# Optimization experiments

Hardware: AMD Instinct MI355X
Metric: run time of the kernel (lower is better)

The kernel has to match this reference:

```python
import jax, jax.numpy as jnp
import numpy as np

N = 100000
E = 1600000
B = 4
IN_C, HID_C, OUT_C = 128, 16, 64
EPS = 1e-5


def _xavier(key, shape):
    fan_in, fan_out = shape[0], shape[1]
    a = float(np.sqrt(6.0 / (fan_in + fan_out)))
    return jax.random.uniform(key, shape, jnp.float32, -a, a)


def setup_inputs() -> dict:
    key = jax.random.key(0)
    ks = jax.random.split(key, 12)
    return {
        "X": jax.random.normal(ks[0], (B, N, IN_C), jnp.float32),
        "edge_index0": jax.random.randint(ks[1], (2, E), 0, N, jnp.int32),
        "edge_weight0": jax.random.uniform(ks[2], (E,), jnp.float32),
        "edge_index1": jax.random.randint(ks[3], (2, E), 0, N, jnp.int32),
        "edge_weight1": jax.random.uniform(ks[4], (E,), jnp.float32),
        "n_id": jnp.arange(N, dtype=jnp.int32),
        "res_n_id0": jnp.arange(N, dtype=jnp.int32),
        "res_n_id1": jnp.arange(N, dtype=jnp.int32),
        # layer 1 params
        "W1_1": _xavier(ks[5], (IN_C, HID_C)),
        "W2_1": _xavier(ks[6], (1, HID_C)),
        "U1": _xavier(ks[7], (HID_C, HID_C)),
        "V1": _xavier(ks[8], (HID_C, HID_C)),
        # layer 2 params
        "W1_2": _xavier(ks[9], (HID_C, OUT_C)),
        "W2_2": _xavier(ks[10], (1, OUT_C)),
        "U2": _xavier(ks[11], (OUT_C, OUT_C)),
        "V2": _xavier(jax.random.fold_in(key, 99), (OUT_C, OUT_C)),
    }


def gated_gcn(x, edge_index, edge_weight, res_n_id, W1, W2, U, V, n_dst):
    # x: [B, N_src, C_in]
    x = x @ W1                                   # [B, N_src, C]
    edge_emb = edge_weight[:, None] * W2[0]      # [E, C]  (edge_feature @ W2)
    src, dst = edge_index[0], edge_index[1]
    msg = edge_emb[None, :, :] * (x[:, src, :] @ V)          # [B, E, C]
    # scatter-mean over destination nodes
    sums = jax.ops.segment_sum(jnp.swapaxes(msg, 0, 1), dst,
                               num_segments=n_dst)            # [N_dst, B, C]
    cnt = jax.ops.segment_sum(jnp.ones((msg.shape[1],), msg.dtype), dst,
                              num_segments=n_dst)
    aggr = jnp.swapaxes(sums, 0, 1) / jnp.maximum(cnt, 1.0)[None, :, None]
    # update
    xr = x[:, res_n_id, :]                       # [B, N_dst, C]
    a = xr @ U + aggr
    # fresh BatchNorm1d(num_features=N_dst) in train mode: normalize each
    # node index over (batch, channel); affine is identity (gamma=1, beta=0)
    mean = jnp.mean(a, axis=(0, 2), keepdims=True)
    var = jnp.var(a, axis=(0, 2), keepdims=True)
    a = jax.nn.relu((a - mean) * jax.lax.rsqrt(var + EPS))
    return xr + a


def reference(X, edge_index0, edge_weight0, edge_index1, edge_weight1,
              n_id, res_n_id0, res_n_id1,
              W1_1, W2_1, U1, V1, W1_2, W2_2, U2, V2):
    X = X[:, n_id, :]
    X = gated_gcn(X, edge_index0, edge_weight0, res_n_id0,
                  W1_1, W2_1, U1, V1, N)
    X = gated_gcn(X, edge_index1, edge_weight1, res_n_id1,
                  W1_2, W2_2, U2, V2, N)
    return X
```

## Files before the change

kernel.cpp:

```cpp
#include <hip/hip_runtime.h>

#define NN 100000
#define EE 1600000
#define EPS 1e-5f
#define NBUK 391
#define NB1 782

typedef __attribute__((ext_vector_type(8))) short short8;
typedef __attribute__((ext_vector_type(4))) float floatx4;
union FragU { uint u[4]; short8 s; };

__device__ __forceinline__ ushort f2bf(float f) {
    uint u = __float_as_uint(f);
    uint r = (u + 0x7FFF + ((u >> 16) & 1)) >> 16;
    return (ushort)r;
}
__device__ __forceinline__ float bf2f(ushort u) {
    return __uint_as_float(((uint)u) << 16);
}

__global__ __launch_bounds__(256) void prep(const float* __restrict__ W1_1,
                                            const float* __restrict__ U1,
                                            const float* __restrict__ V1,
                                            const float* __restrict__ W2_1,
                                            ushort* __restrict__ pack1,
                                            ushort* __restrict__ pack3) {
    int t = threadIdx.x;
    if (blockIdx.x == 0) {
        for (int i = t; i < 2048; i += 256) {
            int e = i & 7, l = (i >> 3) & 63, s = i >> 9;
            pack1[i] = f2bf(W1_1[(s * 32 + ((l >> 4) & 3) * 8 + e) * 16 + (l & 15)]);
        }
    } else {
        for (int i = t; i < 512; i += 256) {
            int e = i & 7, l = i >> 3;
            int kk = ((l >> 4) & 3) * 8 + e, h = l & 15;
            float v = (kk < 16) ? U1[kk * 16 + h] : V1[(kk - 16) * 16 + h] * W2_1[h];
            pack3[i] = f2bf(v);
        }
    }
}

__global__ __launch_bounds__(256) void k1(const float* __restrict__ X,
                                          const ushort* __restrict__ pack1,
                                          ushort* __restrict__ x1g) {
    __shared__ __align__(16) float Xs[64][132];
    int t = threadIdx.x;
    int w = t >> 6, lane = t & 63;
    int nb = blockIdx.x * 16;
#pragma unroll
    for (int i = 0; i < 8; ++i) {
        int flat = i * 256 + t;
        int n_loc = flat >> 7;
        int b = (flat >> 5) & 3;
        int c4 = (flat & 31) << 2;
        float4 v = *reinterpret_cast<const float4*>(&X[((long)b * NN + (nb + n_loc)) * 128 + c4]);
        *reinterpret_cast<float4*>(&Xs[n_loc * 4 + b][c4]) = v;
    }
    __syncthreads();
    int arow = lane & 15, q = lane >> 4;
    floatx4 acc = {0.f, 0.f, 0.f, 0.f};
#pragma unroll
    for (int s = 0; s < 4; ++s) {
        const float* xp = &Xs[w * 16 + arow][s * 32 + q * 8];
        float4 xa = *reinterpret_cast<const float4*>(xp);
        float4 xb = *reinterpret_cast<const float4*>(xp + 4);
        FragU a;
        a.u[0] = ((uint)f2bf(xa.y) << 16) | f2bf(xa.x);
        a.u[1] = ((uint)f2bf(xa.w) << 16) | f2bf(xa.z);
        a.u[2] = ((uint)f2bf(xb.y) << 16) | f2bf(xb.x);
        a.u[3] = ((uint)f2bf(xb.w) << 16) | f2bf(xb.z);
        short8 bfrag = *reinterpret_cast<const short8*>(&pack1[(s * 64 + lane) * 8]);
        acc = __builtin_amdgcn_mfma_f32_16x16x32_bf16(a.s, bfrag, acc, 0, 0, 0);
    }
    int nw = nb + w * 4;
#pragma unroll
    for (int r = 0; r < 4; ++r) {
        int i = q * 4 + r;
        x1g[(long)(nw + (i >> 2)) * 64 + (i & 3) * 16 + (lane & 15)] = f2bf(acc[r]);
    }
}

__global__ __launch_bounds__(256) void passA(const int* __restrict__ ei0,
                                             const int* __restrict__ ei1,
                                             int* __restrict__ bh) {
    int l = blockIdx.x >= NB1;
    int b = blockIdx.x - l * NB1;
    const int* dst = (l ? ei1 : ei0) + EE;
    __shared__ int hist[NBUK];
    int t = threadIdx.x;
    for (int i = t; i < NBUK; i += 256) hist[i] = 0;
    __syncthreads();
    long base = (long)b * 2048;
#pragma unroll
    for (int k = 0; k < 8; ++k) {
        long i = base + k * 256 + t;
        if (i < EE) atomicAdd(&hist[dst[i] >> 8], 1);
    }
    __syncthreads();
    int* bhl = bh + (long)l * NBUK * NB1;
    for (int h = t; h < NBUK; h += 256) bhl[h * NB1 + b] = hist[h];
}

__global__ __launch_bounds__(256) void passB(int* __restrict__ bh, int* __restrict__ colsum) {
    int l = blockIdx.x >= NBUK;
    int h = blockIdx.x - l * NBUK;
    int* row = bh + ((long)l * NBUK + h) * NB1;
    int t = threadIdx.x;
    int v[4];
    int s = 0;
    int b0 = t * 4;
#pragma unroll
    for (int j = 0; j < 4; ++j) {
        int b = b0 + j;
        int x = (b < NB1) ? row[b] : 0;
        v[j] = x;
        s += x;
    }
    int lane = t & 63, wv = t >> 6;
    int x = s;
#pragma unroll
    for (int off = 1; off < 64; off <<= 1) {
        int y = __shfl_up(x, off, 64);
        if (lane >= off) x += y;
    }
    __shared__ int wsum[4], wpre[4];
    if (lane == 63) wsum[wv] = x;
    __syncthreads();
    if (t == 0) {
        int ss = 0;
        for (int i = 0; i < 4; ++i) { wpre[i] = ss; ss += wsum[i]; }
    }
    __syncthreads();
    int run = wpre[wv] + x - s;
#pragma unroll
    for (int j = 0; j < 4; ++j) {
        int b = b0 + j;
        if (b < NB1) row[b] = run;
        run += v[j];
    }
    if (t == 255) colsum[l * NBUK + h] = run;
}

__global__ __launch_bounds__(256) void gbscan(const int* __restrict__ colsum, int* __restrict__ gb,
                                              const float* __restrict__ W1_2,
                                              const float* __restrict__ U2,
                                              const float* __restrict__ V2,
                                              const float* __restrict__ W2_2,
                                              ushort* __restrict__ pack5a,
                                              ushort* __restrict__ pack5b,
                                              int2* __restrict__ ecsr0, int2* __restrict__ ecsr1,
                                              int* __restrict__ rp0, int* __restrict__ rp1) {
    int t = threadIdx.x;
    if (blockIdx.x == 2) {
        for (int i = t; i < 1024; i += 256) {
            int k = i >> 6, j = i & 63;
            float su = 0.f, sv = 0.f;
            for (int m = 0; m < 64; ++m) {
                float wm = W1_2[k * 64 + m];
                su += wm * U2[m * 64 + j];
                sv += wm * V2[m * 64 + j];
            }
            sv *= W2_2[j];
            int jt = j >> 4;
            int l1 = (k >> 3) * 16 + (j & 15);
            int l2 = (2 + (k >> 3)) * 16 + (j & 15);
            int e = k & 7;
            pack5a[(jt * 64 + l1) * 8 + e] = f2bf(su);
            pack5a[(jt * 64 + l2) * 8 + e] = f2bf(sv);
            pack5b[(jt * 64 + l1) * 8 + e] = f2bf(W1_2[k * 64 + j]);
            pack5b[(jt * 64 + l2) * 8 + e] = 0;
        }
        if (t < 16) { ecsr0[EE + t] = make_int2(0, 0); ecsr1[EE + t] = make_int2(0, 0); }
        if (t == 16) rp0[NN] = EE;
        if (t == 17) rp1[NN] = EE;
        return;
    }
    int l = blockIdx.x;
    const int* cs = colsum + l * NBUK;
    int v[2];
    int s = 0;
#pragma unroll
    for (int j = 0; j < 2; ++j) {
        int i = t * 2 + j;
        int x = (i < NBUK) ? cs[i] : 0;
        v[j] = x;
        s += x;
    }
    int lane = t & 63, wv = t >> 6;
    int x = s;
#pragma unroll
    for (int off = 1; off < 64; off <<= 1) {
        int y = __shfl_up(x, off, 64);
        if (lane >= off) x += y;
    }
    __shared__ int wsum[4], wpre[4];
    if (lane == 63) wsum[wv] = x;
    __syncthreads();
    if (t == 0) {
        int ss = 0;
        for (int i = 0; i < 4; ++i) { wpre[i] = ss; ss += wsum[i]; }
    }
    __syncthreads();
    int run = wpre[wv] + x - s;
    int* g = gb + l * 392;
#pragma unroll
    for (int j = 0; j < 2; ++j) {
        int i = t * 2 + j;
        if (i < NBUK) g[i] = run;
        run += v[j];
    }
    if (t == 255) g[NBUK] = run;
}

__global__ __launch_bounds__(256) void passC(const int* __restrict__ ei0, const float* __restrict__ ew0,
                                             const int* __restrict__ ei1, const float* __restrict__ ew1,
                                             const int* __restrict__ bh, const int* __restrict__ gb,
                                             int2* __restrict__ tmp) {
    int l = blockIdx.x >= NB1;
    int b = blockIdx.x - l * NB1;
    const int* ei = l ? ei1 : ei0;
    const float* ew = l ? ew1 : ew0;
    const int* dst = ei + EE;
    __shared__ int cur[NBUK];
    int t = threadIdx.x;
    const int* bhl = bh + (long)l * NBUK * NB1;
    const int* gbl = gb + l * 392;
    for (int h = t; h < NBUK; h += 256) cur[h] = gbl[h] + bhl[h * NB1 + b];
    __syncthreads();
    long base = (long)b * 2048;
    int2* tl = tmp + (long)l * EE;
#pragma unroll
    for (int k = 0; k < 8; ++k) {
        long i = base + k * 256 + t;
        if (i < EE) {
            int d = dst[i];
            int slot = atomicAdd(&cur[d >> 8], 1);
            tl[slot] = make_int2(ei[i] | ((d & 255) << 17), __float_as_int(ew[i]));
        }
    }
}

__global__ __launch_bounds__(256) void passD(const int* __restrict__ gb,
                                             const int2* __restrict__ tmp,
                                             int2* __restrict__ ecsr0, int2* __restrict__ ecsr1,
                                             int* __restrict__ rp0, int* __restrict__ rp1) {
    int l = blockIdx.x >= NBUK;
    int h = blockIdx.x - l * NBUK;
    const int* gbl = gb + l * 392;
    int base = gbl[h], size = gbl[h + 1] - base;
    const int2* tl = tmp + (long)l * EE;
    int2* ecsr = l ? ecsr1 : ecsr0;
    int* rp = l ? rp1 : rp0;
    __shared__ int2 stage[6400];
    __shared__ int hist[256];
    __shared__ int wsum[4], wpre[4];
    int t = threadIdx.x;
    hist[t] = 0;
    __syncthreads();
    bool fit = (size <= 6400);
    for (int i = t; i < size; i += 256) {
        int2 r = tl[base + i];
        if (fit) stage[i] = r;
        atomicAdd(&hist[(r.x >> 17) & 255], 1);
    }
    __syncthreads();
    int v = hist[t];
    int lane = t & 63, wv = t >> 6;
    int x = v;
#pragma unroll
    for (int off = 1; off < 64; off <<= 1) {
        int y = __shfl_up(x, off, 64);
        if (lane >= off) x += y;
    }
    if (lane == 63) wsum[wv] = x;
    __syncthreads();
    if (t == 0) {
        int ss = 0;
        for (int i = 0; i < 4; ++i) { wpre[i] = ss; ss += wsum[i]; }
    }
    __syncthreads();
    int excl = wpre[wv] + x - v;
    int node = h * 256 + t;
    if (node < NN) rp[node] = base + excl;
    __syncthreads();
    hist[t] = excl;
    __syncthreads();
    for (int i = t; i < size; i += 256) {
        int2 r = fit ? stage[i] : tl[base + i];
        int L = (r.x >> 17) & 255;
        int slot = base + atomicAdd(&hist[L], 1);
        ecsr[slot] = make_int2((r.x & 0x1FFFF) << 7, r.y);
    }
}

__global__ __launch_bounds__(256) void k3(const ushort* __restrict__ x1g,
                                          const int2* __restrict__ ecsr0,
                                          const int* __restrict__ rp0,
                                          const ushort* __restrict__ pack3,
                                          ushort* __restrict__ h1g) {
    __shared__ ushort xg[4][16][40];
    int t = threadIdx.x;
    int w = t >> 6, lane = t & 63;
    int b = lane >> 4;
    int nb = blockIdx.x * 16 + w * 4;
    const char* xb = (const char*)x1g;
    int lb = lane << 1;
    for (int nl = 0; nl < 4; ++nl) {
        int n = nb + nl;
        ushort xr16 = x1g[(long)n * 64 + lane];
        int start = rp0[n], end = rp0[n + 1];
        float acc = 0.f;
        int e = start;
        int efull = start + ((end - start) & ~15);
        for (; e < efull; e += 16) {
            int2 r[16];
#pragma unroll
            for (int i = 0; i < 16; ++i) r[i] = ecsr0[e + i];
            float v[16];
#pragma unroll
            for (int i = 0; i < 16; ++i)
                v[i] = bf2f(*(const ushort*)(xb + (uint)r[i].x + lb));
#pragma unroll
            for (int i = 0; i < 16; ++i) acc += __int_as_float(r[i].y) * v[i];
        }
        if (e < end) {
            int2 r[16];
#pragma unroll
            for (int i = 0; i < 16; ++i) r[i] = ecsr0[e + i];
            float v[16];
#pragma unroll
            for (int i = 0; i < 16; ++i)
                v[i] = bf2f(*(const ushort*)(xb + (uint)r[i].x + lb));
#pragma unroll
            for (int i = 0; i < 16; ++i) {
                float wm = (e + i < end) ? __int_as_float(r[i].y) : 0.f;
                acc += wm * v[i];
            }
        }
        float invc = 1.f / fmaxf((float)(end - start), 1.f);
        xg[w][nl * 4 + b][lane & 15] = xr16;
        xg[w][nl * 4 + b][16 + (lane & 15)] = f2bf(acc * invc);
    }
    short8 afrag = *reinterpret_cast<const short8*>(&xg[w][lane & 15][(lane >> 4) * 8]);
    short8 bfrag = *reinterpret_cast<const short8*>(&pack3[lane * 8]);
    floatx4 a4 = {0.f, 0.f, 0.f, 0.f};
    a4 = __builtin_amdgcn_mfma_f32_16x16x32_bf16(afrag, bfrag, a4, 0, 0, 0);
    float s = 0.f, s2 = 0.f;
#pragma unroll
    for (int r = 0; r < 4; ++r) { s += a4[r]; s2 += a4[r] * a4[r]; }
#pragma unroll
    for (int off = 1; off <= 8; off <<= 1) {
        s += __shfl_xor(s, off, 64);
        s2 += __shfl_xor(s2, off, 64);
    }
    float mean = s * (1.f / 64.f);
    float var = s2 * (1.f / 64.f) - mean * mean;
    float rs = rsqrtf(var + EPS);
    int node = lane >> 4;
#pragma unroll
    for (int r = 0; r < 4; ++r) {
        float xv = bf2f(xg[w][node * 4 + r][lane & 15]);
        float hv = xv + fmaxf((a4[r] - mean) * rs, 0.f);
        h1g[(long)(nb + node) * 64 + r * 16 + (lane & 15)] = f2bf(hv);
    }
}

__global__ __launch_bounds__(256) void k5(const ushort* __restrict__ h1g,
                                          const int2* __restrict__ ecsr1,
                                          const int* __restrict__ rp1,
                                          const ushort* __restrict__ pack5a,
                                          const ushort* __restrict__ pack5b,
                                          float* __restrict__ out) {
    __shared__ ushort hg[4][16][40];
    int t = threadIdx.x;
    int w = t >> 6, lane = t & 63;
    int b = lane >> 4;
    int nb = blockIdx.x * 16 + w * 4;
    const char* hb = (const char*)h1g;
    int lb = lane << 1;
    for (int nl = 0; nl < 4; ++nl) {
        int n = nb + nl;
        ushort hv16 = h1g[(long)n * 64 + lane];
        int start = rp1[n], end = rp1[n + 1];
        float acc = 0.f;
        int e = start;
        int efull = start + ((end - start) & ~15);
        for (; e < efull; e += 16) {
            int2 r[16];
#pragma unroll
            for (int i = 0; i < 16; ++i) r[i] = ecsr1[e + i];
            float v[16];
#pragma unroll
            for (int i = 0; i < 16; ++i)
                v[i] = bf2f(*(const ushort*)(hb + (uint)r[i].x + lb));
#pragma unroll
            for (int i = 0; i < 16; ++i) acc += __int_as_float(r[i].y) * v[i];
        }
        if (e < end) {
            int2 r[16];
#pragma unroll
            for (int i = 0; i < 16; ++i) r[i] = ecsr1[e + i];
            float v[16];
#pragma unroll
            for (int i = 0; i < 16; ++i)
                v[i] = bf2f(*(const ushort*)(hb + (uint)r[i].x + lb));
#pragma unroll
            for (int i = 0; i < 16; ++i) {
                float wm = (e + i < end) ? __int_as_float(r[i].y) : 0.f;
                acc += wm * v[i];
            }
        }
        float invc = 1.f / fmaxf((float)(end - start), 1.f);
        hg[w][nl * 4 + b][lane & 15] = hv16;
        hg[w][nl * 4 + b][16 + (lane & 15)] = f2bf(acc * invc);
    }
    short8 afrag = *reinterpret_cast<const short8*>(&hg[w][lane & 15][(lane >> 4) * 8]);
    floatx4 c1[4], c2[4];
#pragma unroll
    for (int jt = 0; jt < 4; ++jt) {
        short8 b1 = *reinterpret_cast<const short8*>(&pack5a[(jt * 64 + lane) * 8]);
        short8 b2 = *reinterpret_cast<const short8*>(&pack5b[(jt * 64 + lane) * 8]);
        floatx4 z = {0.f, 0.f, 0.f, 0.f};
        c1[jt] = __builtin_amdgcn_mfma_f32_16x16x32_bf16(afrag, b1, z, 0, 0, 0);
        c2[jt] = __builtin_amdgcn_mfma_f32_16x16x32_bf16(afrag, b2, z, 0, 0, 0);
    }
    float s = 0.f, s2 = 0.f;
#pragma unroll
    for (int jt = 0; jt < 4; ++jt)
#pragma unroll
        for (int r = 0; r < 4; ++r) { float a = c1[jt][r]; s += a; s2 += a * a; }
#pragma unroll
    for (int off = 1; off <= 8; off <<= 1) {
        s += __shfl_xor(s, off, 64);
        s2 += __shfl_xor(s2, off, 64);
    }
    float mean = s * (1.f / 256.f);
    float var = s2 * (1.f / 256.f) - mean * mean;
    float rs = rsqrtf(var + EPS);
    int node = lane >> 4;
    long n = nb + node;
#pragma unroll
    for (int r = 0; r < 4; ++r)
#pragma unroll
        for (int jt = 0; jt < 4; ++jt) {
            float norm = (c1[jt][r] - mean) * rs;
            out[((long)r * NN + n) * 64 + jt * 16 + (lane & 15)] = c2[jt][r] + fmaxf(norm, 0.f);
        }
}

extern "C" void kernel_launch(void* const* d_in, const int* in_sizes, int n_in,
                              void* d_out, int out_size, void* d_ws, size_t ws_size,
                              hipStream_t stream) {
    const float* X    = (const float*)d_in[0];
    const int*   ei0  = (const int*)d_in[1];
    const float* ew0  = (const float*)d_in[2];
    const int*   ei1  = (const int*)d_in[3];
    const float* ew1  = (const float*)d_in[4];
    const float* W1_1 = (const float*)d_in[8];
    const float* W2_1 = (const float*)d_in[9];
    const float* U1   = (const float*)d_in[10];
    const float* V1   = (const float*)d_in[11];
    const float* W1_2 = (const float*)d_in[12];
    const float* W2_2 = (const float*)d_in[13];
    const float* U2   = (const float*)d_in[14];
    const float* V2   = (const float*)d_in[15];
    float* out = (float*)d_out;
    char* ws = (char*)d_ws;

    const long MB = 1000000L;
    ushort* x1g   = (ushort*)(ws + 0L);
    ushort* h1g   = (ushort*)(ws + 13 * MB);
    int2*   tmp   = (int2*)(ws + 26 * MB);
    int*    bh    = (int*)(ws + 52 * MB);
    int*    colsum= (int*)(ws + 55 * MB);
    int*    gb    = (int*)(ws + 55 * MB + 4096);
    int*    rp0   = (int*)(ws + 56 * MB);
    int*    rp1   = (int*)(ws + 57 * MB);
    int2*   ecsr0 = (int2*)(ws + 58 * MB);
    int2*   ecsr1 = (int2*)(ws + 71 * MB);
    ushort* pack1  = (ushort*)(ws + 84 * MB);
    ushort* pack3  = (ushort*)(ws + 84 * MB + 8192);
    ushort* pack5a = (ushort*)(ws + 84 * MB + 16384);
    ushort* pack5b = (ushort*)(ws + 84 * MB + 24576);

    prep<<<2, 256, 0, stream>>>(W1_1, U1, V1, W2_1, pack1, pack3);
    k1<<<6250, 256, 0, stream>>>(X, pack1, x1g);
    passA<<<2 * NB1, 256, 0, stream>>>(ei0, ei1, bh);
    passB<<<2 * NBUK, 256, 0, stream>>>(bh, colsum);
    gbscan<<<3, 256, 0, stream>>>(colsum, gb, W1_2, U2, V2, W2_2, pack5a, pack5b,
                                  ecsr0, ecsr1, rp0, rp1);
    passC<<<2 * NB1, 256, 0, stream>>>(ei0, ew0, ei1, ew1, bh, gb, tmp);
    passD<<<2 * NBUK, 256, 0, stream>>>(gb, tmp, ecsr0, ecsr1, rp0, rp1);
    k3<<<6250, 256, 0, stream>>>(x1g, ecsr0, rp0, pack3, h1g);
    k5<<<6250, 256, 0, stream>>>(h1g, ecsr1, rp1, pack5a, pack5b, out);
}
```

Before: 347.5 us.

## Fuse prep, k1 and histogram pass; merge per-node edge loops in gathers

Merges the weight-packing prep kernel and the destination-histogram pass into the first projection kernel as extra blocks, and moves the pack3 weight prep into the gbscan launch. This removes two launches and lets the histogram blocks overlap with the dense projection. In k3 and k5, each wave now walks the contiguous edge range of its four nodes as one loop, routing each product to the right node with predicated accumulates, which removes per-node tail loops and partial batches. In exchange, every k1 block recomputes the W1_1 bf16 packing into shared memory, and the gather loop adds compare-and-select work per edge.

Measured after the change: 328.1 us. 5.6% less time.

```diff
diff --git a/kernel.cpp b/kernel.cpp
--- a/kernel.cpp
+++ b/kernel.cpp
@@ -5,6 +5,7 @@
 #define EPS 1e-5f
 #define NBUK 391
 #define NB1 782
+#define K1B 6250
 
 typedef __attribute__((ext_vector_type(8))) short short8;
 typedef __attribute__((ext_vector_type(4))) float floatx4;
@@ -19,35 +20,41 @@
     return __uint_as_float(((uint)u) << 16);
 }
 
-__global__ __launch_bounds__(256) void prep(const float* __restrict__ W1_1,
-                                            const float* __restrict__ U1,
-                                            const float* __restrict__ V1,
-                                            const float* __restrict__ W2_1,
-                                            ushort* __restrict__ pack1,
-                                            ushort* __restrict__ pack3) {
-    int t = threadIdx.x;
-    if (blockIdx.x == 0) {
-        for (int i = t; i < 2048; i += 256) {
-            int e = i & 7, l = (i >> 3) & 63, s = i >> 9;
-            pack1[i] = f2bf(W1_1[(s * 32 + ((l >> 4) & 3) * 8 + e) * 16 + (l & 15)]);
-        }
-    } else {
-        for (int i = t; i < 512; i += 256) {
-            int e = i & 7, l = i >> 3;
-            int kk = ((l >> 4) & 3) * 8 + e, h = l & 15;
-            float v = (kk < 16) ? U1[kk * 16 + h] : V1[(kk - 16) * 16 + h] * W2_1[h];
-            pack3[i] = f2bf(v);
-        }
-    }
-}
-
-__global__ __launch_bounds__(256) void k1(const float* __restrict__ X,
-                                          const ushort* __restrict__ pack1,
-                                          ushort* __restrict__ x1g) {
-    __shared__ __align__(16) float Xs[64][132];
-    int t = threadIdx.x;
+__global__ __launch_bounds__(256) void kA(const float* __restrict__ X,
+                                          const float* __restrict__ W1_1,
+                                          ushort* __restrict__ x1g,
+                                          const int* __restrict__ ei0,
+                                          const int* __restrict__ ei1,
+                                          int* __restrict__ bh) {
+    __shared__ __align__(16) char smem[64 * 132 * 4 + 4096];
+    int t = threadIdx.x;
+    if (blockIdx.x >= K1B) {
+        int bp = blockIdx.x - K1B;
+        int l = bp >= NB1;
+        int b = bp - l * NB1;
+        const int* dst = (l ? ei1 : ei0) + EE;
+        int* hist = (int*)smem;
+        for (int i = t; i < NBUK; i += 256) hist[i] = 0;
+        __syncthreads();
+        long base = (long)b * 2048;
+#pragma unroll
+        for (int k = 0; k < 8; ++k) {
+            long i = base + k * 256 + t;
+            if (i < EE) atomicAdd(&hist[dst[i] >> 8], 1);
+        }
+        __syncthreads();
+        int* bhl = bh + (long)l * NBUK * NB1;
+        for (int h = t; h < NBUK; h += 256) bhl[h * NB1 + b] = hist[h];
+        return;
+    }
+    float (*Xs)[132] = (float(*)[132])smem;
+    ushort* Ws = (ushort*)(smem + 64 * 132 * 4);
     int w = t >> 6, lane = t & 63;
     int nb = blockIdx.x * 16;
+    for (int i = t; i < 2048; i += 256) {
+        int e = i & 7, l = (i >> 3) & 63, s = i >> 9;
+        Ws[i] = f2bf(W1_1[(s * 32 + ((l >> 4) & 3) * 8 + e) * 16 + (l & 15)]);
+    }
 #pragma unroll
     for (int i = 0; i < 8; ++i) {
         int flat = i * 256 + t;
@@ -70,7 +77,7 @@
         a.u[1] = ((uint)f2bf(xa.w) << 16) | f2bf(xa.z);
         a.u[2] = ((uint)f2bf(xb.y) << 16) | f2bf(xb.x);
         a.u[3] = ((uint)f2bf(xb.w) << 16) | f2bf(xb.z);
-        short8 bfrag = *reinterpret_cast<const short8*>(&pack1[(s * 64 + lane) * 8]);
+        short8 bfrag = *reinterpret_cast<const short8*>(&Ws[(s * 64 + lane) * 8]);
         acc = __builtin_amdgcn_mfma_f32_16x16x32_bf16(a.s, bfrag, acc, 0, 0, 0);
     }
     int nw = nb + w * 4;
@@ -79,27 +86,6 @@
         int i = q * 4 + r;
         x1g[(long)(nw + (i >> 2)) * 64 + (i & 3) * 16 + (lane & 15)] = f2bf(acc[r]);
     }
-}
-
-__global__ __launch_bounds__(256) void passA(const int* __restrict__ ei0,
-                                             const int* __restrict__ ei1,
-                                             int* __restrict__ bh) {
-    int l = blockIdx.x >= NB1;
-    int b = blockIdx.x - l * NB1;
-    const int* dst = (l ? ei1 : ei0) + EE;
-    __shared__ int hist[NBUK];
-    int t = threadIdx.x;
-    for (int i = t; i < NBUK; i += 256) hist[i] = 0;
-    __syncthreads();
-    long base = (long)b * 2048;
-#pragma unroll
-    for (int k = 0; k < 8; ++k) {
-        long i = base + k * 256 + t;
-        if (i < EE) atomicAdd(&hist[dst[i] >> 8], 1);
-    }
-    __syncthreads();
-    int* bhl = bh + (long)l * NBUK * NB1;
-    for (int h = t; h < NBUK; h += 256) bhl[h * NB1 + b] = hist[h];
 }
 
 __global__ __launch_bounds__(256) void passB(int* __restrict__ bh, int* __restrict__ colsum) {
@@ -147,11 +133,24 @@
                                               const float* __restrict__ U2,
                                               const float* __restrict__ V2,
                                               const float* __restrict__ W2_2,
+                                              const float* __restrict__ U1,
+                                              const float* __restrict__ V1,
+                                              const float* __restrict__ W2_1,
                                               ushort* __restrict__ pack5a,
                                               ushort* __restrict__ pack5b,
+                                              ushort* __restrict__ pack3,
                                               int2* __restrict__ ecsr0, int2* __restrict__ ecsr1,
                                               int* __restrict__ rp0, int* __restrict__ rp1) {
     int t = threadIdx.x;
+    if (blockIdx.x == 3) {
+        for (int i = t; i < 512; i += 256) {
+            int e = i & 7, l = i >> 3;
+            int kk = ((l >> 4) & 3) * 8 + e, h = l & 15;
+            float v = (kk < 16) ? U1[kk * 16 + h] : V1[(kk - 16) * 16 + h] * W2_1[h];
+            pack3[i] = f2bf(v);
+        }
+        return;
+    }
     if (blockIdx.x == 2) {
         for (int i = t; i < 1024; i += 256) {
             int k = i >> 6, j = i & 63;
@@ -306,42 +305,35 @@
     int nb = blockIdx.x * 16 + w * 4;
     const char* xb = (const char*)x1g;
     int lb = lane << 1;
-    for (int nl = 0; nl < 4; ++nl) {
-        int n = nb + nl;
-        ushort xr16 = x1g[(long)n * 64 + lane];
-        int start = rp0[n], end = rp0[n + 1];
-        float acc = 0.f;
-        int e = start;
-        int efull = start + ((end - start) & ~15);
-        for (; e < efull; e += 16) {
-            int2 r[16];
-#pragma unroll
-            for (int i = 0; i < 16; ++i) r[i] = ecsr0[e + i];
-            float v[16];
-#pragma unroll
-            for (int i = 0; i < 16; ++i)
-                v[i] = bf2f(*(const ushort*)(xb + (uint)r[i].x + lb));
-#pragma unroll
-            for (int i = 0; i < 16; ++i) acc += __int_as_float(r[i].y) * v[i];
-        }
-        if (e < end) {
-            int2 r[16];
-#pragma unroll
-            for (int i = 0; i < 16; ++i) r[i] = ecsr0[e + i];
-            float v[16];
-#pragma unroll
-            for (int i = 0; i < 16; ++i)
-                v[i] = bf2f(*(const ushort*)(xb + (uint)r[i].x + lb));
-#pragma unroll
-            for (int i = 0; i < 16; ++i) {
-                float wm = (e + i < end) ? __int_as_float(r[i].y) : 0.f;
-                acc += wm * v[i];
-            }
-        }
-        float invc = 1.f / fmaxf((float)(end - start), 1.f);
-        xg[w][nl * 4 + b][lane & 15] = xr16;
-        xg[w][nl * 4 + b][16 + (lane & 15)] = f2bf(acc * invc);
-    }
+    int s0 = rp0[nb], b1 = rp0[nb + 1], b2 = rp0[nb + 2], b3 = rp0[nb + 3], s4 = rp0[nb + 4];
+    float acc0 = 0.f, acc1 = 0.f, acc2 = 0.f, acc3 = 0.f;
+    for (int e = s0; e < s4; e += 16) {
+        int2 r[16];
+#pragma unroll
+        for (int i = 0; i < 16; ++i) r[i] = ecsr0[e + i];
+        float v[16];
+#pragma unroll
+        for (int i = 0; i < 16; ++i)
+            v[i] = bf2f(*(const ushort*)(xb + (uint)r[i].x + lb));
+#pragma unroll
+        for (int i = 0; i < 16; ++i) {
+            int gi = e + i;
+            float wm = (gi < s4) ? __int_as_float(r[i].y) : 0.f;
+            float c = wm * v[i];
+            acc0 += (gi < b1) ? c : 0.f;
+            acc1 += (gi >= b1 && gi < b2) ? c : 0.f;
+            acc2 += (gi >= b2 && gi < b3) ? c : 0.f;
+            acc3 += (gi >= b3) ? c : 0.f;
+        }
+    }
+    int h = lane & 15;
+    xg[w][0 * 4 + b][16 + h] = f2bf(acc0 / fmaxf((float)(b1 - s0), 1.f));
+    xg[w][1 * 4 + b][16 + h] = f2bf(acc1 / fmaxf((float)(b2 - b1), 1.f));
+    xg[w][2 * 4 + b][16 + h] = f2bf(acc2 / fmaxf((float)(b3 - b2), 1.f));
+    xg[w][3 * 4 + b][16 + h] = f2bf(acc3 / fmaxf((float)(s4 - b3), 1.f));
+#pragma unroll
+    for (int j = 0; j < 4; ++j)
+        xg[w][j * 4 + b][h] = x1g[(long)(nb + j) * 64 + lane];
     short8 afrag = *reinterpret_cast<const short8*>(&xg[w][lane & 15][(lane >> 4) * 8]);
     short8 bfrag = *reinterpret_cast<const short8*>(&pack3[lane * 8]);
     floatx4 a4 = {0.f, 0.f, 0.f, 0.f};
@@ -379,51 +371,44 @@
     int nb = blockIdx.x * 16 + w * 4;
     const char* hb = (const char*)h1g;
     int lb = lane << 1;
-    for (int nl = 0; nl < 4; ++nl) {
-        int n = nb + nl;
-        ushort hv16 = h1g[(long)n * 64 + lane];
-        int start = rp1[n], end = rp1[n + 1];
-        float acc = 0.f;
-        int e = start;
-        int efull = start + ((end - start) & ~15);
-        for (; e < efull; e += 16) {
-            int2 r[16];
-#pragma unroll
-            for (int i = 0; i < 16; ++i) r[i] = ecsr1[e + i];
-            float v[16];
-#pragma unroll
-            for (int i = 0; i < 16; ++i)
-                v[i] = bf2f(*(const ushort*)(hb + (uint)r[i].x + lb));
-#pragma unroll
-            for (int i = 0; i < 16; ++i) acc += __int_as_float(r[i].y) * v[i];
-        }
-        if (e < end) {
-            int2 r[16];
-#pragma unroll
-            for (int i = 0; i < 16; ++i) r[i] = ecsr1[e + i];
-            float v[16];
-#pragma unroll
-            for (int i = 0; i < 16; ++i)
-                v[i] = bf2f(*(const ushort*)(hb + (uint)r[i].x + lb));
-#pragma unroll
-            for (int i = 0; i < 16; ++i) {
-                float wm = (e + i < end) ? __int_as_float(r[i].y) : 0.f;
-                acc += wm * v[i];
-            }
-        }
-        float invc = 1.f / fmaxf((float)(end - start), 1.f);
-        hg[w][nl * 4 + b][lane & 15] = hv16;
-        hg[w][nl * 4 + b][16 + (lane & 15)] = f2bf(acc * invc);
-    }
+    int s0 = rp1[nb], b1 = rp1[nb + 1], b2 = rp1[nb + 2], b3 = rp1[nb + 3], s4 = rp1[nb + 4];
+    float acc0 = 0.f, acc1 = 0.f, acc2 = 0.f, acc3 = 0.f;
+    for (int e = s0; e < s4; e += 16) {
+        int2 r[16];
+#pragma unroll
+        for (int i = 0; i < 16; ++i) r[i] = ecsr1[e + i];
+        float v[16];
+#pragma unroll
+        for (int i = 0; i < 16; ++i)
+            v[i] = bf2f(*(const ushort*)(hb + (uint)r[i].x + lb));
+#pragma unroll
+        for (int i = 0; i < 16; ++i) {
+            int gi = e + i;
+            float wm = (gi < s4) ? __int_as_float(r[i].y) : 0.f;
+            float c = wm * v[i];
+            acc0 += (gi < b1) ? c : 0.f;
+            acc1 += (gi >= b1 && gi < b2) ? c : 0.f;
+            acc2 += (gi >= b2 && gi < b3) ? c : 0.f;
+            acc3 += (gi >= b3) ? c : 0.f;
+        }
+    }
+    int h = lane & 15;
+    hg[w][0 * 4 + b][16 + h] = f2bf(acc0 / fmaxf((float)(b1 - s0), 1.f));
+    hg[w][1 * 4 + b][16 + h] = f2bf(acc1 / fmaxf((float)(b2 - b1), 1.f));
+    hg[w][2 * 4 + b][16 + h] = f2bf(acc2 / fmaxf((float)(b3 - b2), 1.f));
+    hg[w][3 * 4 + b][16 + h] = f2bf(acc3 / fmaxf((float)(s4 - b3), 1.f));
+#pragma unroll
+    for (int j = 0; j < 4; ++j)
+        hg[w][j * 4 + b][h] = h1g[(long)(nb + j) * 64 + lane];
     short8 afrag = *reinterpret_cast<const short8*>(&hg[w][lane & 15][(lane >> 4) * 8]);
     floatx4 c1[4], c2[4];
 #pragma unroll
     for (int jt = 0; jt < 4; ++jt) {
-        short8 b1 = *reinterpret_cast<const short8*>(&pack5a[(jt * 64 + lane) * 8]);
-        short8 b2 = *reinterpret_cast<const short8*>(&pack5b[(jt * 64 + lane) * 8]);
+        short8 bb1 = *reinterpret_cast<const short8*>(&pack5a[(jt * 64 + lane) * 8]);
+        short8 bb2 = *reinterpret_cast<const short8*>(&pack5b[(jt * 64 + lane) * 8]);
         floatx4 z = {0.f, 0.f, 0.f, 0.f};
-        c1[jt] = __builtin_amdgcn_mfma_f32_16x16x32_bf16(afrag, b1, z, 0, 0, 0);
-        c2[jt] = __builtin_amdgcn_mfma_f32_16x16x32_bf16(afrag, b2, z, 0, 0, 0);
+        c1[jt] = __builtin_amdgcn_mfma_f32_16x16x32_bf16(afrag, bb1, z, 0, 0, 0);
+        c2[jt] = __builtin_amdgcn_mfma_f32_16x16x32_bf16(afrag, bb2, z, 0, 0, 0);
     }
     float s = 0.f, s2 = 0.f;
 #pragma unroll
@@ -479,19 +464,16 @@
     int*    rp1   = (int*)(ws + 57 * MB);
     int2*   ecsr0 = (int2*)(ws + 58 * MB);
     int2*   ecsr1 = (int2*)(ws + 71 * MB);
-    ushort* pack1  = (ushort*)(ws + 84 * MB);
-    ushort* pack3  = (ushort*)(ws + 84 * MB + 8192);
-    ushort* pack5a = (ushort*)(ws + 84 * MB + 16384);
-    ushort* pack5b = (ushort*)(ws + 84 * MB + 24576);
-
-    prep<<<2, 256, 0, stream>>>(W1_1, U1, V1, W2_1, pack1, pack3);
-    k1<<<6250, 256, 0, stream>>>(X, pack1, x1g);
-    passA<<<2 * NB1, 256, 0, stream>>>(ei0, ei1, bh);
+    ushort* pack3  = (ushort*)(ws + 84 * MB);
+    ushort* pack5a = (ushort*)(ws + 84 * MB + 8192);
+    ushort* pack5b = (ushort*)(ws + 84 * MB + 16384);
+
+    kA<<<K1B + 2 * NB1, 256, 0, stream>>>(X, W1_1, x1g, ei0, ei1, bh);
     passB<<<2 * NBUK, 256, 0, stream>>>(bh, colsum);
-    gbscan<<<3, 256, 0, stream>>>(colsum, gb, W1_2, U2, V2, W2_2, pack5a, pack5b,
-                                  ecsr0, ecsr1, rp0, rp1);
+    gbscan<<<4, 256, 0, stream>>>(colsum, gb, W1_2, U2, V2, W2_2, U1, V1, W2_1,
+                                  pack5a, pack5b, pack3, ecsr0, ecsr1, rp0, rp1);
     passC<<<2 * NB1, 256, 0, stream>>>(ei0, ew0, ei1, ew1, bh, gb, tmp);
     passD<<<2 * NBUK, 256, 0, stream>>>(gb, tmp, ecsr0, ecsr1, rp0, rp1);
-    k3<<<6250, 256, 0, stream>>>(x1g, ecsr0, rp0, pack3, h1g);
-    k5<<<6250, 256, 0, stream>>>(h1g, ecsr1, rp1, pack5a, pack5b, out);
-}
+    k3<<<K1B, 256, 0, stream>>>(x1g, ecsr0, rp0, pack3, h1g);
+    k5<<<K1B, 256, 0, stream>>>(h1g, ecsr1, rp1, pack5a, pack5b, out);
+}
```
